# Optimization experiments

Hardware: AMD Instinct MI355X
Metric: run time of the kernel (lower is better)

Reference implementation:

```python
import jax, jax.numpy as jnp
import numpy as np

HEADS = 16
C = 256  # number_clusters


def setup_inputs() -> dict:
    key = jax.random.key(0)
    ks = jax.random.split(key, 6)
    b, n, d = 8, 4096, 1024
    q = jax.random.normal(ks[0], (b, n, d), jnp.float32)
    cluster = jax.random.randint(ks[1], (b, n), 0, C)
    s = 1.0 / np.sqrt(d)
    w_q = jax.random.normal(ks[2], (d, d), jnp.float32) * s
    w_kv = jax.random.normal(ks[3], (d, 2 * d), jnp.float32) * s
    w_proj = jax.random.normal(ks[4], (d, d), jnp.float32) * s
    b_proj = jnp.zeros((d,), jnp.float32)
    return {"cluster": cluster, "q": q, "w_q": w_q, "w_kv": w_kv,
            "w_proj": w_proj, "b_proj": b_proj}


def _forward(cluster, x, w_q, w_kv, w_proj, b_proj):
    b, n, d = x.shape
    h = HEADS
    dh = d // h
    # projections
    qh = (x @ w_q).reshape(b, n, h, dh).transpose(0, 2, 1, 3)          # b h n dh
    kv = (x @ w_kv).reshape(b, n, 2, h, dh).transpose(2, 0, 3, 1, 4)   # 2 b h n dh
    k, v = kv[0], kv[1]
    # cluster segment-mean of k and v (CalcCenter with weights = 1/count)
    onehot = jax.nn.one_hot(cluster, C, dtype=x.dtype)                 # b n C
    counts = onehot.sum(axis=1)                                        # b C
    inv = jnp.where(counts > 0, 1.0 / counts, 0.0)                     # b C
    k_center = jnp.einsum('bnc,bhnd->bhcd', onehot, k) * inv[:, None, :, None]
    v_center = jnp.einsum('bnc,bhnd->bhcd', onehot, v) * inv[:, None, :, None]
    # attention over cluster centers
    score = jnp.einsum('bhnd,bhcd->bhnc', qh, k_center) / jnp.sqrt(jnp.asarray(dh, x.dtype))
    attn = jax.nn.softmax(score, axis=-1)                              # softmax_temp = 1
    # count-weighted softmax renormalization (WeightedSoftMax with weight=k_counts)
    attn = attn * counts[:, None, None, :]
    attn = attn / attn.sum(axis=-1, keepdims=True)
    out = jnp.einsum('bhnc,bhcd->bhnd', attn, v_center)                # b h n dh
    out = out.transpose(0, 2, 1, 3).reshape(b, n, d)
    return out @ w_proj + b_proj


def reference(cluster, q, w_q, w_kv, w_proj, b_proj):
    return _forward(cluster, q, w_q, w_kv, w_proj, b_proj)
```

## Files before the change

kernel.cpp:

```cpp
#include <hip/hip_runtime.h>
#include <hip/hip_bf16.h>
#include <math.h>

#define HEADS 16
#define NCL 256
#define BB 8
#define NN 4096
#define DD 1024
#define DH 64
#define MM (BB*NN)
#define KK 1024

typedef unsigned short u16;
typedef __attribute__((ext_vector_type(8))) short s8v;
typedef __attribute__((ext_vector_type(4))) float f32x4;

__device__ __forceinline__ float bf2f(u16 u) {
    union { unsigned int i; float f; } v; v.i = ((unsigned int)u) << 16; return v.f;
}
__device__ __forceinline__ u16 f2bf(float x) {
    union { float f; unsigned int i; } v; v.f = x;
    unsigned int u = v.i;
    return (u16)((u + 0x7FFFu + ((u >> 16) & 1u)) >> 16);
}
__device__ __forceinline__ unsigned int pk2hi(unsigned int a, unsigned int b) {
    return __builtin_amdgcn_perm(b, a, 0x07060302);
}
__device__ __forceinline__ void gl16(const u16* g, u16* l) {
    __builtin_amdgcn_global_load_lds(
        (__attribute__((address_space(1))) void*)g,
        (__attribute__((address_space(3))) void*)l, 16, 0, 0);
}

__global__ __launch_bounds__(256) void prep_k(const int* __restrict__ cluster,
                                              int* __restrict__ counts,
                                              float2* __restrict__ tab,
                                              int* __restrict__ tokidx,
                                              int* __restrict__ starts) {
    __shared__ int cl[NN];
    __shared__ int pf[NCL];
    const int bb = blockIdx.x;
    const int tid = threadIdx.x;

    pf[tid] = 0;
    __syncthreads();
    for (int i = tid; i < NN; i += 256) {
        int c = cluster[bb * NN + i];
        cl[i] = c;
        atomicAdd(&pf[c], 1);
    }
    __syncthreads();

    const int myc = pf[tid];
    counts[bb * NCL + tid] = myc;
    float2 t;
    t.x = myc > 0 ? 0.125f / (float)myc : 0.f;
    t.y = (float)myc;
    tab[bb * NCL + tid] = t;

    for (int off = 1; off < NCL; off <<= 1) {
        int v = (tid >= off) ? pf[tid - off] : 0;
        __syncthreads();
        pf[tid] += v;
        __syncthreads();
    }
    int start = pf[tid] - myc;
    starts[bb * NCL + tid] = start;

    int* dst = tokidx + bb * NN + start;
    int rank = 0;
    for (int t0 = 0; t0 < NN; t0 += 16) {
        int c16[16];
#pragma unroll
        for (int j = 0; j < 16; ++j) c16[j] = cl[t0 + j];
#pragma unroll
        for (int j = 0; j < 16; ++j) {
            if (c16[j] == tid) { dst[rank] = t0 + j; ++rank; }
        }
    }
}

__global__ __launch_bounds__(256) void convx1_k(const float* __restrict__ x,
                                                u16* __restrict__ hi) {
    size_t i = ((size_t)blockIdx.x * 256 + threadIdx.x) * 4;
    float4 v = *(const float4*)(x + i);
    ushort4 h;
    h.x = f2bf(v.x); h.y = f2bf(v.y); h.z = f2bf(v.z); h.w = f2bf(v.w);
    *(ushort4*)(hi + i) = h;
}

__global__ __launch_bounds__(256) void convw3_k(const float* __restrict__ wq,
                                                const float* __restrict__ wkv,
                                                const float* __restrict__ wproj,
                                                u16* __restrict__ thi,
                                                u16* __restrict__ tlo) {
    __shared__ float t[32][33];
    const int wz = blockIdx.z;
    const int bx = blockIdx.x, by = blockIdx.y;
    const int N = (wz == 1) ? 2048 : 1024;
    if (bx * 32 >= N) return;
    const float* w = (wz == 0) ? wq : (wz == 1) ? wkv : wproj;
    const size_t nbase = (wz == 0) ? 0 : (wz == 1) ? 1024 : 3072;
    const int lx = threadIdx.x & 31, ly = threadIdx.x >> 5;
#pragma unroll
    for (int p = 0; p < 4; ++p)
        t[p * 8 + ly][lx] = w[(size_t)(by * 32 + p * 8 + ly) * N + bx * 32 + lx];
    __syncthreads();
#pragma unroll
    for (int p = 0; p < 4; ++p) {
        size_t n = nbase + bx * 32 + p * 8 + ly;
        int k = by * 32 + lx;
        float v = t[lx][p * 8 + ly];
        u16 h = f2bf(v);
        thi[n * KK + k] = h;
        tlo[n * KK + k] = f2bf(v - bf2f(h));
    }
}

__global__ __launch_bounds__(256) void xsum2_k(const float* __restrict__ x,
                                               const int* __restrict__ tokidx,
                                               const int* __restrict__ starts,
                                               const int* __restrict__ counts,
                                               u16* __restrict__ shi,
                                               u16* __restrict__ slo) {
    const int bb = blockIdx.x >> 8;
    const int c = blockIdx.x & (NCL - 1);
    const int tid = threadIdx.x;
    const int start = starts[bb * NCL + c];
    const int cnt = counts[bb * NCL + c];
    const int* ti = tokidx + bb * NN + start;

    float a[4] = {0.f, 0.f, 0.f, 0.f};
    for (int i = 0; i < cnt; ++i) {
        int t = ti[i];
        const float* xr = x + ((size_t)bb * NN + t) * DD;
#pragma unroll
        for (int j = 0; j < 4; ++j) a[j] += xr[tid + 256 * j];
    }
    size_t o = ((size_t)bb * NCL + c) * DD;
#pragma unroll
    for (int j = 0; j < 4; ++j) {
        u16 h = f2bf(a[j]);
        shi[o + tid + 256 * j] = h;
        slo[o + tid + 256 * j] = f2bf(a[j] - bf2f(h));
    }
}

__global__ __launch_bounds__(256) void convk_k(const float* __restrict__ Csum,
                                               u16* __restrict__ khi) {
    const int bh = blockIdx.x;
    const int bb = bh >> 4, hh = bh & 15;
    const int tid = threadIdx.x;
#pragma unroll
    for (int i = 0; i < 8; ++i) {
        int ulin = tid + 256 * i;
        int c = ulin >> 3, u = ulin & 7;
        const float* src = Csum + ((size_t)(bb * NCL + c)) * 2048 + hh * 64 + u * 8;
        float4 v0 = *(const float4*)src;
        float4 v1 = *(const float4*)(src + 4);
        size_t o = ((size_t)bh * NCL + c) * 64 + ((u ^ (c & 7)) << 3);
        ushort4 h0, h1;
        h0.x = f2bf(v0.x); h0.y = f2bf(v0.y); h0.z = f2bf(v0.z); h0.w = f2bf(v0.w);
        h1.x = f2bf(v1.x); h1.y = f2bf(v1.y); h1.z = f2bf(v1.z); h1.w = f2bf(v1.w);
        *(ushort4*)(khi + o) = h0; *(ushort4*)(khi + o + 4) = h1;
    }
}

__global__ __launch_bounds__(256) void convv_k(const float* __restrict__ Csum,
                                               u16* __restrict__ vthi,
                                               u16* __restrict__ vtlo) {
    __shared__ float vb[NCL][65];
    const int bh = blockIdx.x;
    const int bb = bh >> 4, hh = bh & 15;
    const int tid = threadIdx.x;
    const int d0 = tid & 63;
#pragma unroll
    for (int i = 0; i < 64; ++i) {
        int c = (tid >> 6) + i * 4;
        vb[c][d0] = Csum[((size_t)(bb * NCL + c)) * 2048 + 1024 + hh * 64 + d0];
    }
    __syncthreads();
    const int d = tid >> 2;
    const int uq = tid & 3;
#pragma unroll
    for (int j = 0; j < 8; ++j) {
        int u = uq * 8 + j;
        int c0 = u * 8;
        float v[8];
#pragma unroll
        for (int e = 0; e < 8; ++e) v[e] = vb[c0 + e][d];
        ushort4 h0, l0, h1, l1;
        h0.x = f2bf(v[0]); l0.x = f2bf(v[0] - bf2f(h0.x));
        h0.y = f2bf(v[1]); l0.y = f2bf(v[1] - bf2f(h0.y));
        h0.z = f2bf(v[2]); l0.z = f2bf(v[2] - bf2f(h0.z));
        h0.w = f2bf(v[3]); l0.w = f2bf(v[3] - bf2f(h0.w));
        h1.x = f2bf(v[4]); l1.x = f2bf(v[4] - bf2f(h1.x));
        h1.y = f2bf(v[5]); l1.y = f2bf(v[5] - bf2f(h1.y));
        h1.z = f2bf(v[6]); l1.z = f2bf(v[6] - bf2f(h1.z));
        h1.w = f2bf(v[7]); l1.w = f2bf(v[7] - bf2f(h1.w));
        int usw = (u & 24) | ((u ^ d) & 7);
        size_t o = ((size_t)bh * 64 + d) * 256 + usw * 8;
        *(ushort4*)(vthi + o) = h0; *(ushort4*)(vthi + o + 4) = h1;
        *(ushort4*)(vtlo + o) = l0; *(ushort4*)(vtlo + o + 4) = l1;
    }
}

template<int OUT>
__global__ __launch_bounds__(256) void hgemm_k(
        const u16* __restrict__ Ahi, const u16* __restrict__ Alo,
        const u16* __restrict__ Bhi, const u16* __restrict__ Blo,
        float* __restrict__ C, int ldc, const float* __restrict__ bias,
        u16* __restrict__ Ohi, u16* __restrict__ Olo) {
    __shared__ u16 sh[4][128 * 32];

    const int tid = threadIdx.x;
    const int lane = tid & 63;
    const int wid = tid >> 6;
    const int wm = wid >> 1, wn = wid & 1;
    const size_t row0 = (size_t)blockIdx.y * 128;
    const size_t col0 = (size_t)blockIdx.x * 128;

    const int sr = tid >> 2;
    const int sq = tid & 3;
    const int qs = sq ^ ((sr >> 1) & 3);

    const u16* ga0 = Ahi + (row0 + sr) * KK + qs * 8;
    const u16* ga1 = ga0 + (size_t)64 * KK;
    const u16* gA0 = Alo + (row0 + sr) * KK + qs * 8;
    const u16* gA1 = gA0 + (size_t)64 * KK;
    const u16* gb0 = Bhi + (col0 + sr) * KK + qs * 8;
    const u16* gb1 = gb0 + (size_t)64 * KK;
    const u16* gB0 = Blo + (col0 + sr) * KK + qs * 8;
    const u16* gB1 = gB0 + (size_t)64 * KK;

    u16* d = (u16*)sh + tid * 8;

    const int rA = wm * 64 + (lane & 15);
    const int rB = wn * 64 + (lane & 15);
    const int aoff = rA * 32 + (((lane >> 4) ^ ((rA >> 1) & 3)) * 8);
    const int boff = rB * 32 + (((lane >> 4) ^ ((rB >> 1) & 3)) * 8);

    f32x4 acc[4][4] = {};

    for (int k0 = 0; k0 < KK; k0 += 32) {
        gl16(ga0 + k0, d);
        gl16(ga1 + k0, d + 2048);
        gl16(gA0 + k0, d + 4096);
        gl16(gA1 + k0, d + 6144);
        gl16(gb0 + k0, d + 8192);
        gl16(gb1 + k0, d + 10240);
        gl16(gB0 + k0, d + 12288);
        gl16(gB1 + k0, d + 14336);
        __syncthreads();
        s8v ah[4], al[4], bh[4], bl[4];
#pragma unroll
        for (int i = 0; i < 4; ++i) {
            ah[i] = *(const s8v*)&sh[0][aoff + i * 512];
            al[i] = *(const s8v*)&sh[1][aoff + i * 512];
            bh[i] = *(const s8v*)&sh[2][boff + i * 512];
            bl[i] = *(const s8v*)&sh[3][boff + i * 512];
        }
#pragma unroll
        for (int i = 0; i < 4; ++i)
#pragma unroll
            for (int j = 0; j < 4; ++j) {
                acc[i][j] = __builtin_amdgcn_mfma_f32_16x16x32_bf16(ah[i], bh[j], acc[i][j], 0, 0, 0);
                acc[i][j] = __builtin_amdgcn_mfma_f32_16x16x32_bf16(ah[i], bl[j], acc[i][j], 0, 0, 0);
                acc[i][j] = __builtin_amdgcn_mfma_f32_16x16x32_bf16(al[i], bh[j], acc[i][j], 0, 0, 0);
            }
        __syncthreads();
    }

    const int fr = (lane >> 4) * 4;
    const int fc = lane & 15;

    float bj[4] = {0.f, 0.f, 0.f, 0.f};
    if constexpr (OUT == 1) {
#pragma unroll
        for (int j = 0; j < 4; ++j) bj[j] = bias[col0 + wn * 64 + j * 16 + fc];
    }
#pragma unroll
    for (int i = 0; i < 4; ++i)
#pragma unroll
        for (int j = 0; j < 4; ++j) {
            size_t rbase = row0 + wm * 64 + i * 16 + fr;
            size_t cidx = col0 + wn * 64 + j * 16 + fc;
#pragma unroll
            for (int g = 0; g < 4; ++g)
                C[(rbase + g) * (size_t)ldc + cidx] = acc[i][j][g] + bj[j];
        }
}

template<int OUT, int SGL>
__global__ __launch_bounds__(512) void hgemm256_k(
        const u16* __restrict__ Ahi, const u16* __restrict__ Alo,
        const u16* __restrict__ Bhi, const u16* __restrict__ Blo,
        float* __restrict__ C, int ldc, const float* __restrict__ bias,
        u16* __restrict__ Ohi, u16* __restrict__ Olo) {
    __shared__ u16 sh[2][4][8192];

    const int tid = threadIdx.x;
    const int lane = tid & 63;
    const int wid = tid >> 6;
    const int wm = wid >> 2, wn = wid & 3;
    const int l15 = lane & 15;

    const int nwg = gridDim.x;
    const int cpx = nwg >> 3;
    const int lin = blockIdx.x;
    const int swz = (lin & 7) * cpx + (lin >> 3);
    const int bx = swz & 3;
    const int by = swz >> 2;

    const size_t row0 = (size_t)by * 256;
    const size_t col0 = (size_t)bx * 256;

    const int sr0 = tid >> 2;
    const int qs0 = (tid & 3) ^ ((sr0 >> 1) & 3);
    const u16* pAh0 = Ahi + (row0 + sr0) * KK + qs0 * 8;
    const u16* pAh1 = pAh0 + (size_t)128 * KK;
    const u16* pAl0 = Alo + (row0 + sr0) * KK + qs0 * 8;
    const u16* pAl1 = pAl0 + (size_t)128 * KK;
    const u16* pBh0 = Bhi + (col0 + sr0) * KK + qs0 * 8;
    const u16* pBh1 = pBh0 + (size_t)128 * KK;
    const u16* pBl0 = Blo + (col0 + sr0) * KK + qs0 * 8;
    const u16* pBl1 = pBl0 + (size_t)128 * KK;

#define STG_A(bw, k) { u16* db = (u16*)sh + (bw) * 32768 + tid * 8;            \
        gl16(pAh0 + (k), db);            gl16(pAh1 + (k), db + 4096);          \
        if constexpr (!SGL) {                                                  \
            gl16(pAl0 + (k), db + 8192); gl16(pAl1 + (k), db + 12288); } }
#define STG_B(bw, k) { u16* db = (u16*)sh + (bw) * 32768 + 16384 + tid * 8;    \
        gl16(pBh0 + (k), db);            gl16(pBh1 + (k), db + 4096);          \
        if constexpr (!SGL) {                                                  \
            gl16(pBl0 + (k), db + 8192); gl16(pBl1 + (k), db + 12288); } }

    const int rA = wm * 128 + l15;
    const int rB = wn * 64 + l15;
    const int aoff = rA * 32 + (((lane >> 4) ^ ((rA >> 1) & 3)) * 8);
    const int boff = rB * 32 + (((lane >> 4) ^ ((rB >> 1) & 3)) * 8);

    f32x4 acc[8][4] = {};

    STG_A(0, 0);
    STG_B(0, 0);
    __syncthreads();

    int cur = 0;
    for (int kt = 0; kt < 32; ++kt) {
        const int kn = (kt + 1) * 32;
        const u16* br = (const u16*)sh + cur * 32768;
        const int bw = cur ^ 1;
        const bool st = kt < 31;

        if constexpr (SGL) {
            if (st) { STG_A(bw, kn); STG_B(bw, kn); }
            s8v bhf[4];
#pragma unroll
            for (int ni = 0; ni < 4; ++ni)
                bhf[ni] = *(const s8v*)(br + 16384 + boff + ni * 512);
            s8v ahf[8];
#pragma unroll
            for (int mi = 0; mi < 8; ++mi)
                ahf[mi] = *(const s8v*)(br + aoff + mi * 512);
            __builtin_amdgcn_s_setprio(1);
#pragma unroll
            for (int mi = 0; mi < 8; ++mi)
#pragma unroll
                for (int ni = 0; ni < 4; ++ni)
                    acc[mi][ni] = __builtin_amdgcn_mfma_f32_16x16x32_bf16(ahf[mi], bhf[ni], acc[mi][ni], 0, 0, 0);
            __builtin_amdgcn_s_setprio(0);
            __syncthreads();
            cur ^= 1;
            continue;
        }

        if (st) STG_A(bw, kn);
        s8v bhf[4], blf[4];
#pragma unroll
        for (int ni = 0; ni < 4; ++ni) {
            bhf[ni] = *(const s8v*)(br + 16384 + boff + ni * 512);
            blf[ni] = *(const s8v*)(br + 24576 + boff + ni * 512);
        }
        {
            s8v ah0 = *(const s8v*)(br + aoff);
            s8v al0 = *(const s8v*)(br + 8192 + aoff);
            s8v ah1 = *(const s8v*)(br + aoff + 512);
            s8v al1 = *(const s8v*)(br + 8192 + aoff + 512);
            __builtin_amdgcn_s_setprio(1);
#pragma unroll
            for (int ni = 0; ni < 4; ++ni) {
                acc[0][ni] = __builtin_amdgcn_mfma_f32_16x16x32_bf16(ah0, bhf[ni], acc[0][ni], 0, 0, 0);
                acc[0][ni] = __builtin_amdgcn_mfma_f32_16x16x32_bf16(ah0, blf[ni], acc[0][ni], 0, 0, 0);
                acc[0][ni] = __builtin_amdgcn_mfma_f32_16x16x32_bf16(al0, bhf[ni], acc[0][ni], 0, 0, 0);
                acc[1][ni] = __builtin_amdgcn_mfma_f32_16x16x32_bf16(ah1, bhf[ni], acc[1][ni], 0, 0, 0);
                acc[1][ni] = __builtin_amdgcn_mfma_f32_16x16x32_bf16(ah1, blf[ni], acc[1][ni], 0, 0, 0);
                acc[1][ni] = __builtin_amdgcn_mfma_f32_16x16x32_bf16(al1, bhf[ni], acc[1][ni], 0, 0, 0);
            }
            __builtin_amdgcn_s_setprio(0);
        }
        __builtin_amdgcn_s_barrier();

#pragma unroll
        for (int p = 1; p < 4; ++p) {
            if (p == 1 && st) STG_B(bw, kn);
            const int m0 = 2 * p;
            s8v ah0 = *(const s8v*)(br + aoff + m0 * 512);
            s8v al0 = *(const s8v*)(br + 8192 + aoff + m0 * 512);
            s8v ah1 = *(const s8v*)(br + aoff + (m0 + 1) * 512);
            s8v al1 = *(const s8v*)(br + 8192 + aoff + (m0 + 1) * 512);
            __builtin_amdgcn_s_setprio(1);
#pragma unroll
            for (int ni = 0; ni < 4; ++ni) {
                acc[m0][ni] = __builtin_amdgcn_mfma_f32_16x16x32_bf16(ah0, bhf[ni], acc[m0][ni], 0, 0, 0);
                acc[m0][ni] = __builtin_amdgcn_mfma_f32_16x16x32_bf16(ah0, blf[ni], acc[m0][ni], 0, 0, 0);
                acc[m0][ni] = __builtin_amdgcn_mfma_f32_16x16x32_bf16(al0, bhf[ni], acc[m0][ni], 0, 0, 0);
                acc[m0 + 1][ni] = __builtin_amdgcn_mfma_f32_16x16x32_bf16(ah1, bhf[ni], acc[m0 + 1][ni], 0, 0, 0);
                acc[m0 + 1][ni] = __builtin_amdgcn_mfma_f32_16x16x32_bf16(ah1, blf[ni], acc[m0 + 1][ni], 0, 0, 0);
                acc[m0 + 1][ni] = __builtin_amdgcn_mfma_f32_16x16x32_bf16(al1, bhf[ni], acc[m0 + 1][ni], 0, 0, 0);
            }
            __builtin_amdgcn_s_setprio(0);
            if (p < 3) __builtin_amdgcn_s_barrier();
        }

        __syncthreads();
        cur ^= 1;
    }
#undef STG_A
#undef STG_B

    const int fr = (lane >> 4) * 4;
    const int fc = lane & 15;

    if constexpr (OUT == 2) {
#pragma unroll
        for (int mi = 0; mi < 8; ++mi)
#pragma unroll
            for (int ni = 0; ni < 4; ++ni) {
                size_t rbase = row0 + wm * 128 + mi * 16 + fr;
                size_t cidx = col0 + wn * 64 + ni * 16 + fc;
#pragma unroll
                for (int g = 0; g < 4; ++g) {
                    float o = acc[mi][ni][g];
                    u16 h = f2bf(o);
                    size_t idx = (rbase + g) * 1024 + cidx;
                    Ohi[idx] = h;
                    if constexpr (!SGL) {
                        Olo[idx] = f2bf(o - bf2f(h));
                    }
                }
            }
    } else {
        float bj[4];
#pragma unroll
        for (int ni = 0; ni < 4; ++ni) bj[ni] = bias[col0 + wn * 64 + ni * 16 + fc];
#pragma unroll
        for (int mi = 0; mi < 8; ++mi)
#pragma unroll
            for (int ni = 0; ni < 4; ++ni) {
                size_t rbase = row0 + wm * 128 + mi * 16 + fr;
                size_t cidx = col0 + wn * 64 + ni * 16 + fc;
#pragma unroll
                for (int g = 0; g < 4; ++g)
                    C[(rbase + g) * (size_t)ldc + cidx] = acc[mi][ni][g] + bj[ni];
            }
    }
}

__global__ __launch_bounds__(256) void fattn_k(const u16* __restrict__ Qhi,
                                               const u16* __restrict__ Khi,
                                               const u16* __restrict__ Vthi,
                                               const u16* __restrict__ Vtlo,
                                               const float2* __restrict__ tab,
                                               u16* __restrict__ Phi,
                                               u16* __restrict__ Plo) {
    __shared__ u16 qh[64 * 64];
    __shared__ u16 zb[16 * 512];
    __shared__ float lpart[4][64];
    __shared__ float invl[64];

    const int tid = threadIdx.x;
    const int lane = tid & 63;
    const int w = tid >> 6;
    const int g = lane >> 4;
    const int l15 = lane & 15;
    const int hh = blockIdx.y, bb = blockIdx.z;
    const int bh = bb * 16 + hh;
    const int tok0 = blockIdx.x * 64;

#pragma unroll
    for (int i = 0; i < 2; ++i) {
        int ulin = tid + 256 * i;
        int tok = ulin >> 3, up = ulin & 7;
        size_t src = ((size_t)(bb * NN + tok0 + tok)) * 1024 + hh * 64
                     + ((up ^ (tok & 7)) << 3);
        gl16(Qhi + src, qh + ulin * 8);
    }
    __syncthreads();

    const size_t kbase = (size_t)bh * NCL * 64;
    const size_t vbase = (size_t)bh * 64 * 256;
    const int dg = w * 16 + l15;

    float lp[4] = {0.f, 0.f, 0.f, 0.f};
    f32x4 oacc[4] = {};

#pragma unroll
    for (int h = 0; h < 2; ++h) {
        f32x4 acch[2][4] = {};
#pragma unroll
        for (int ff = 0; ff < 2; ++ff) {
            const int f = 2 * h + ff;
            const int cl = w * 64 + f * 16 + l15;
            s8v kf[2];
#pragma unroll
            for (int ks = 0; ks < 2; ++ks) {
                size_t ko = kbase + (size_t)cl * 64 + (((ks * 4 + g) ^ (l15 & 7)) << 3);
                kf[ks] = *(const s8v*)(Khi + ko);
            }
#pragma unroll
            for (int cf = 0; cf < 4; ++cf) {
                const int qr = cf * 16 + l15;
#pragma unroll
                for (int ks = 0; ks < 2; ++ks) {
                    int qa = qr * 64 + (((ks * 4 + g) ^ (qr & 7)) << 3);
                    s8v qfh = *(const s8v*)&qh[qa];
                    acch[ff][cf] = __builtin_amdgcn_mfma_f32_16x16x32_bf16(kf[ks], qfh, acch[ff][cf], 0, 0, 0);
                }
            }
        }

#pragma unroll
        for (int ff = 0; ff < 2; ++ff) {
            const int f = 2 * h + ff;
            float2 t4[4];
#pragma unroll
            for (int r = 0; r < 4; ++r)
                t4[r] = tab[bb * NCL + w * 64 + f * 16 + 4 * g + r];
#pragma unroll
            for (int cf = 0; cf < 4; ++cf) {
                float z[4];
#pragma unroll
                for (int r = 0; r < 4; ++r) {
                    float e = __expf(acch[ff][cf][r] * t4[r].x);
                    lp[cf] += t4[r].y * e;
                    z[r] = t4[r].y > 0.f ? e : 0.f;
                }
                uint2 pz;
                pz.x = (unsigned int)f2bf(z[0]) | ((unsigned int)f2bf(z[1]) << 16);
                pz.y = (unsigned int)f2bf(z[2]) | ((unsigned int)f2bf(z[3]) << 16);
                int a16 = (w * 4 + cf) * 512
                          + ((2 * ff + (g >> 1)) * 16 + l15) * 8 + 4 * (g & 1);
                *(uint2*)&zb[a16] = pz;
            }
        }

        if (h == 1) {
#pragma unroll
            for (int cf = 0; cf < 4; ++cf) {
                float v = lp[cf];
                v += __shfl_xor(v, 16);
                v += __shfl_xor(v, 32);
                lp[cf] = v;
            }
            if (lane < 16) {
#pragma unroll
                for (int cf = 0; cf < 4; ++cf) lpart[w][cf * 16 + lane] = lp[cf];
            }
        }
        __syncthreads();

        if (h == 1 && w == 0)
            invl[lane] = 1.f / (lpart[0][lane] + lpart[1][lane] + lpart[2][lane] + lpart[3][lane]);

#pragma unroll
        for (int s = 0; s < 4; ++s) {
            int kst = 2 * s + h;
            size_t vo = vbase + (size_t)dg * 256
                        + (((kst * 4 + g) & 24) | (((kst * 4 + g) ^ dg) & 7)) * 8;
            s8v vh = *(const s8v*)(Vthi + vo);
            s8v vl = *(const s8v*)(Vtlo + vo);
#pragma unroll
            for (int cf = 0; cf < 4; ++cf) {
                int a16 = (s * 4 + cf) * 512 + lane * 8;
                s8v zf = *(const s8v*)&zb[a16];
                oacc[cf] = __builtin_amdgcn_mfma_f32_16x16x32_bf16(vh, zf, oacc[cf], 0, 0, 0);
                oacc[cf] = __builtin_amdgcn_mfma_f32_16x16x32_bf16(vl, zf, oacc[cf], 0, 0, 0);
            }
        }
        __syncthreads();
    }

#pragma unroll
    for (int cf = 0; cf < 4; ++cf) {
        const int tokL = cf * 16 + l15;
        float il = invl[tokL];
        float o0 = oacc[cf][0] * il, o1 = oacc[cf][1] * il;
        float o2 = oacc[cf][2] * il, o3 = oacc[cf][3] * il;
        unsigned int b0 = __float_as_uint(o0), b1 = __float_as_uint(o1);
        unsigned int b2 = __float_as_uint(o2), b3 = __float_as_uint(o3);
        float r0 = o0 - __uint_as_float(b0 & 0xFFFF0000u);
        float r1 = o1 - __uint_as_float(b1 & 0xFFFF0000u);
        float r2 = o2 - __uint_as_float(b2 & 0xFFFF0000u);
        float r3 = o3 - __uint_as_float(b3 & 0xFFFF0000u);
        uint2 ph, pl;
        ph.x = pk2hi(b0, b1); ph.y = pk2hi(b2, b3);
        pl.x = pk2hi(__float_as_uint(r0), __float_as_uint(r1));
        pl.y = pk2hi(__float_as_uint(r2), __float_as_uint(r3));
        size_t po = ((size_t)(bb * NN + tok0 + tokL)) * 1024 + hh * 64 + w * 16 + 4 * g;
        *(uint2*)(Phi + po) = ph;
        *(uint2*)(Plo + po) = pl;
    }
}

extern "C" void kernel_launch(void* const* d_in, const int* in_sizes, int n_in,
                              void* d_out, int out_size, void* d_ws, size_t ws_size,
                              hipStream_t stream) {
    const int* cluster  = (const int*)d_in[0];
    const float* x      = (const float*)d_in[1];
    const float* w_q    = (const float*)d_in[2];
    const float* w_kv   = (const float*)d_in[3];
    const float* w_proj = (const float*)d_in[4];
    const float* b_proj = (const float*)d_in[5];
    float* out = (float*)d_out;

    const size_t SZ_H  = (size_t)MM * 1024 * 2;
    const size_t SZ_W  = (size_t)4096 * 1024 * 2;
    const size_t SZ_XS = (size_t)2048 * 1024 * 2;
    const size_t SZ_CS = (size_t)2048 * 2048 * 4;
    const size_t SZ_KV = (size_t)128 * NCL * 64 * 2;

    char* p = (char*)d_ws;
    u16* Xhi = (u16*)p;   p += SZ_H;
    u16* Xlo = (u16*)p;   p += SZ_H;
    u16* Qhi = (u16*)p;   p += SZ_H;
    u16* Qlo = (u16*)p;   p += SZ_H;
    u16* Wthi = (u16*)p;  p += SZ_W;
    u16* Wtlo = (u16*)p;  p += SZ_W;
    u16* XShi = (u16*)p;  p += SZ_XS;
    u16* XSlo = (u16*)p;  p += SZ_XS;
    float* Csum = (float*)p; p += SZ_CS;
    u16* Khi = (u16*)p;   p += SZ_KV;
    u16* Klo = (u16*)p;   p += SZ_KV;
    u16* Vthi = (u16*)p;  p += SZ_KV;
    u16* Vtlo = (u16*)p;  p += SZ_KV;
    float2* tab = (float2*)p; p += 2048 * sizeof(float2);
    int* counts = (int*)p;   p += 2048 * sizeof(int);
    int* tokidx = (int*)p;   p += (size_t)BB * NN * sizeof(int);
    int* starts = (int*)p;
    (void)Klo; (void)Qlo;

    prep_k<<<BB, 256, 0, stream>>>(cluster, counts, tab, tokidx, starts);

    convx1_k<<<(size_t)MM * KK / 1024, 256, 0, stream>>>(x, Xhi);
    convw3_k<<<dim3(64, 32, 3), 256, 0, stream>>>(w_q, w_kv, w_proj, Wthi, Wtlo);

    xsum2_k<<<BB * NCL, 256, 0, stream>>>(x, tokidx, starts, counts, XShi, XSlo);

    hgemm256_k<2, 1><<<512, 512, 0, stream>>>(Xhi, Xlo, Wthi, Wtlo,
                                              nullptr, 0, nullptr, Qhi, Qlo);
    hgemm_k<0><<<dim3(16, 16), 256, 0, stream>>>(XShi, XSlo,
                                                 Wthi + (size_t)1024 * KK, Wtlo + (size_t)1024 * KK,
                                                 Csum, 2048, nullptr, nullptr, nullptr);
    convk_k<<<128, 256, 0, stream>>>(Csum, Khi);
    convv_k<<<128, 256, 0, stream>>>(Csum, Vthi, Vtlo);

    fattn_k<<<dim3(NN / 64, HEADS, BB), 256, 0, stream>>>(Qhi, Khi,
                                                          Vthi, Vtlo, tab, Xhi, Xlo);
    hgemm256_k<1, 0><<<512, 512, 0, stream>>>(Xhi, Xlo,
                                              Wthi + (size_t)3072 * KK, Wtlo + (size_t)3072 * KK,
                                              out, 1024, b_proj, nullptr, nullptr);
}
```

Baseline: 583.5 us.

## Fuse fp32-to-bf16 conversion of x into the Q projection GEMM and merge K/V conversion kernels

The Q projection GEMM now loads fp32 x tiles directly into shared memory and converts them to bf16 while building MFMA fragments. This removes the separate convx1_k pass that wrote a bf16 copy of x. The convk and convv kernels are merged into a single launch. In exchange the GEMM stages twice the bytes for the A operand and does extra conversion ALU work in its inner loop.

```diff
diff --git a/kernel.cpp b/kernel.cpp
--- a/kernel.cpp
+++ b/kernel.cpp
@@ -78,15 +78,6 @@
             if (c16[j] == tid) { dst[rank] = t0 + j; ++rank; }
         }
     }
-}
-
-__global__ __launch_bounds__(256) void convx1_k(const float* __restrict__ x,
-                                                u16* __restrict__ hi) {
-    size_t i = ((size_t)blockIdx.x * 256 + threadIdx.x) * 4;
-    float4 v = *(const float4*)(x + i);
-    ushort4 h;
-    h.x = f2bf(v.x); h.y = f2bf(v.y); h.z = f2bf(v.z); h.w = f2bf(v.w);
-    *(ushort4*)(hi + i) = h;
 }
 
 __global__ __launch_bounds__(256) void convw3_k(const float* __restrict__ wq,
@@ -146,11 +137,15 @@
     }
 }
 
-__global__ __launch_bounds__(256) void convk_k(const float* __restrict__ Csum,
-                                               u16* __restrict__ khi) {
+__global__ __launch_bounds__(256) void convkv_k(const float* __restrict__ Csum,
+                                                u16* __restrict__ khi,
+                                                u16* __restrict__ vthi,
+                                                u16* __restrict__ vtlo) {
+    __shared__ float vb[NCL][65];
     const int bh = blockIdx.x;
     const int bb = bh >> 4, hh = bh & 15;
     const int tid = threadIdx.x;
+
 #pragma unroll
     for (int i = 0; i < 8; ++i) {
         int ulin = tid + 256 * i;
@@ -164,15 +159,7 @@
         h1.x = f2bf(v1.x); h1.y = f2bf(v1.y); h1.z = f2bf(v1.z); h1.w = f2bf(v1.w);
         *(ushort4*)(khi + o) = h0; *(ushort4*)(khi + o + 4) = h1;
     }
-}
-
-__global__ __launch_bounds__(256) void convv_k(const float* __restrict__ Csum,
-                                               u16* __restrict__ vthi,
-                                               u16* __restrict__ vtlo) {
-    __shared__ float vb[NCL][65];
-    const int bh = blockIdx.x;
-    const int bb = bh >> 4, hh = bh & 15;
-    const int tid = threadIdx.x;
+
     const int d0 = tid & 63;
 #pragma unroll
     for (int i = 0; i < 64; ++i) {
@@ -291,6 +278,114 @@
         }
 }
 
+__global__ __launch_bounds__(512) void qgemm_k(const float* __restrict__ X,
+                                               const u16* __restrict__ Bhi,
+                                               u16* __restrict__ Ohi) {
+    __shared__ u16 sh2[2][24576];
+
+    const int tid = threadIdx.x;
+    const int lane = tid & 63;
+    const int wid = tid >> 6;
+    const int wm = wid >> 2, wn = wid & 3;
+    const int l15 = lane & 15;
+    const int g = lane >> 4;
+
+    const int nwg = gridDim.x;
+    const int cpx = nwg >> 3;
+    const int lin = blockIdx.x;
+    const int swz = (lin & 7) * cpx + (lin >> 3);
+    const int bx = swz & 3;
+    const int by = swz >> 2;
+
+    const size_t row0 = (size_t)by * 256;
+    const size_t col0 = (size_t)bx * 256;
+
+    const int ra = tid >> 1;
+    const int pa = tid & 1;
+    const int swra = (ra >> 2) & 1;
+    const float* pX[4];
+#pragma unroll
+    for (int c = 0; c < 4; ++c)
+        pX[c] = X + (row0 + ra) * 1024 + (((2 * c + pa) ^ swra) * 4);
+
+    const int sr0 = tid >> 2;
+    const int qs0 = (tid & 3) ^ ((sr0 >> 1) & 3);
+    const u16* pBh0 = Bhi + (col0 + sr0) * KK + qs0 * 8;
+    const u16* pBh1 = pBh0 + (size_t)128 * KK;
+
+#define QSTG(bw, k) {                                                          \
+        u16* ab = sh2[bw];                                                     \
+        gl16((const u16*)(pX[0] + (k)), ab + tid * 8);                         \
+        gl16((const u16*)(pX[1] + (k)), ab + 4096 + tid * 8);                  \
+        gl16((const u16*)(pX[2] + (k)), ab + 8192 + tid * 8);                  \
+        gl16((const u16*)(pX[3] + (k)), ab + 12288 + tid * 8);                 \
+        u16* db = ab + 16384 + tid * 8;                                        \
+        gl16(pBh0 + (k), db);  gl16(pBh1 + (k), db + 4096); }
+
+    const int rB = wn * 64 + l15;
+    const int boff = rB * 32 + (((lane >> 4) ^ ((rB >> 1) & 3)) * 8);
+    const int swl = (l15 >> 2) & 1;
+    const int abyte = g * 8192 + (wm * 128 + l15) * 32 + swl * 16;
+
+    f32x4 acc[8][4] = {};
+
+    QSTG(0, 0);
+    __syncthreads();
+
+    int cur = 0;
+    for (int kt = 0; kt < 32; ++kt) {
+        const int kn = (kt + 1) * 32;
+        const char* Ab = (const char*)sh2[cur];
+        const u16* Bb = sh2[cur] + 16384;
+        const int bw = cur ^ 1;
+        if (kt < 31) QSTG(bw, kn);
+
+        s8v bhf[4];
+#pragma unroll
+        for (int ni = 0; ni < 4; ++ni)
+            bhf[ni] = *(const s8v*)(Bb + boff + ni * 512);
+
+        s8v ahf[8];
+#pragma unroll
+        for (int mi = 0; mi < 8; ++mi) {
+            int b0 = abyte + mi * 512;
+            f32x4 flo = *(const f32x4*)(Ab + b0);
+            f32x4 fhi = *(const f32x4*)(Ab + (b0 ^ 16));
+            uint4 q;
+            q.x = pk2hi(__float_as_uint(flo[0]), __float_as_uint(flo[1]));
+            q.y = pk2hi(__float_as_uint(flo[2]), __float_as_uint(flo[3]));
+            q.z = pk2hi(__float_as_uint(fhi[0]), __float_as_uint(fhi[1]));
+            q.w = pk2hi(__float_as_uint(fhi[2]), __float_as_uint(fhi[3]));
+            union { uint4 u; s8v s; } cv; cv.u = q;
+            ahf[mi] = cv.s;
+        }
+
+        __builtin_amdgcn_s_setprio(1);
+#pragma unroll
+        for (int mi = 0; mi < 8; ++mi)
+#pragma unroll
+            for (int ni = 0; ni < 4; ++ni)
+                acc[mi][ni] = __builtin_amdgcn_mfma_f32_16x16x32_bf16(ahf[mi], bhf[ni], acc[mi][ni], 0, 0, 0);
+        __builtin_amdgcn_s_setprio(0);
+        __syncthreads();
+        cur ^= 1;
+    }
+#undef QSTG
+
+    const int fr = (lane >> 4) * 4;
+    const int fc = lane & 15;
+#pragma unroll
+    for (int mi = 0; mi < 8; ++mi)
+#pragma unroll
+        for (int ni = 0; ni < 4; ++ni) {
+            size_t rbase = row0 + wm * 128 + mi * 16 + fr;
+            size_t cidx = col0 + wn * 64 + ni * 16 + fc;
+#pragma unroll
+            for (int g2 = 0; g2 < 4; ++g2)
+                Ohi[(rbase + g2) * 1024 + cidx] = f2bf(acc[mi][ni][g2]);
+        }
+}
+
 template<int OUT, int SGL>
 __global__ __launch_bounds__(512) void hgemm256_k(
         const u16* __restrict__ Ahi, const u16* __restrict__ Alo,
@@ -352,28 +447,6 @@
         const u16* br = (const u16*)sh + cur * 32768;
         const int bw = cur ^ 1;
         const bool st = kt < 31;
-
-        if constexpr (SGL) {
-            if (st) { STG_A(bw, kn); STG_B(bw, kn); }
-            s8v bhf[4];
-#pragma unroll
-            for (int ni = 0; ni < 4; ++ni)
-                bhf[ni] = *(const s8v*)(br + 16384 + boff + ni * 512);
-            s8v ahf[8];
-#pragma unroll
-            for (int mi = 0; mi < 8; ++mi)
-                ahf[mi] = *(const s8v*)(br + aoff + mi * 512);
-            __builtin_amdgcn_s_setprio(1);
-#pragma unroll
-            for (int mi = 0; mi < 8; ++mi)
-#pragma unroll
-                for (int ni = 0; ni < 4; ++ni)
-                    acc[mi][ni] = __builtin_amdgcn_mfma_f32_16x16x32_bf16(ahf[mi], bhf[ni], acc[mi][ni], 0, 0, 0);
-            __builtin_amdgcn_s_setprio(0);
-            __syncthreads();
-            cur ^= 1;
-            continue;
-        }
 
         if (st) STG_A(bw, kn);
         s8v bhf[4], blf[4];
@@ -652,18 +725,16 @@
 
     prep_k<<<BB, 256, 0, stream>>>(cluster, counts, tab, tokidx, starts);
 
-    convx1_k<<<(size_t)MM * KK / 1024, 256, 0, stream>>>(x, Xhi);
     convw3_k<<<dim3(64, 32, 3), 256, 0, stream>>>(w_q, w_kv, w_proj, Wthi, Wtlo);
 
     xsum2_k<<<BB * NCL, 256, 0, stream>>>(x, tokidx, starts, counts, XShi, XSlo);
 
-    hgemm256_k<2, 1><<<512, 512, 0, stream>>>(Xhi, Xlo, Wthi, Wtlo,
-                                              nullptr, 0, nullptr, Qhi, Qlo);
+    qgemm_k<<<512, 512, 0, stream>>>(x, Wthi, Qhi);
+
     hgemm_k<0><<<dim3(16, 16), 256, 0, stream>>>(XShi, XSlo,
                                                  Wthi + (size_t)1024 * KK, Wtlo + (size_t)1024 * KK,
                                                  Csum, 2048, nullptr, nullptr, nullptr);
-    convk_k<<<128, 256, 0, stream>>>(Csum, Khi);
-    convv_k<<<128, 256, 0, stream>>>(Csum, Vthi, Vtlo);
+    convkv_k<<<128, 256, 0, stream>>>(Csum, Khi, Vthi, Vtlo);
 
     fattn_k<<<dim3(NN / 64, HEADS, BB), 256, 0, stream>>>(Qhi, Khi,
                                                           Vthi, Vtlo, tab, Xhi, Xlo);
```

Result: slower. 595.8 us (+2.1%).
